# Kernel tuning notes

Measured on AMD Instinct MI355X. Metric: run time of the kernel, lower is better.

Reference implementation:

```python
import jax, jax.numpy as jnp
import numpy as np

B, N_NODES, E = 2, 4096, 16384
H, DQK, DV = 8, 16, 128
DV_HEAD = DV // H  # dim_v_head = dim_v // n_heads


def setup_inputs() -> dict:
    key = jax.random.key(0)
    k1, k2, k3, k4, k5 = jax.random.split(key, 5)
    return {
        "query_values": jax.random.normal(k1, (B, E, H * DQK), jnp.float32),
        "key_values": jax.random.normal(k2, (B, N_NODES, H * DQK), jnp.float32),
        "value_values": jax.random.normal(k3, (B, E, DV), jnp.float32),
        "query_indices": jax.random.randint(k4, (B, E, 2), 0, N_NODES, jnp.int32),
        "value_indices": jax.random.randint(k5, (B, E, 2), 0, N_NODES, jnp.int32),
    }


def _heads(x, d):
    # torch: stack(x.split(d, -1), 0)  => [N, H*d] -> [H, N, d], head-major chunks
    n = x.shape[0]
    return jnp.transpose(x.reshape(n, -1, d), (1, 0, 2))


def reference(query_values, key_values, value_values, query_indices, value_indices):
    b, eq, _ = query_values.shape
    n_nodes = key_values.shape[1]
    n = b * n_nodes                       # total nodes across batch
    nv = b * eq                           # total value/query edges (full mask)
    node_ofs = (jnp.arange(b, dtype=query_indices.dtype) * n_nodes)[:, None, None]

    # _concat_batch: masked flatten (mask all True) + per-head split
    q = _heads(query_values.reshape(nv, -1), DQK)       # [H, Nq, d]
    k = _heads(key_values.reshape(n, -1), DQK)          # [H, n,  d]
    v = _heads(value_values.reshape(nv, -1), DV_HEAD)   # [H, Nv, dv_head]

    # _partial_key_value_sum: gather keys at edge row index, outer product, scatter-add by col
    v_idx = (value_indices + node_ofs).reshape(nv, 2)
    row, col = v_idx[:, 0], v_idx[:, 1]
    k_g = k[:, row, :]                                  # [H, Nv, d]
    # cat(unbind(h),-1).flatten(1,2): layout (n, i*DV + h*DV_HEAD + j)
    kv = jnp.einsum('hni,hnj->nihj', k_g, v).reshape(nv, DQK * DV)
    kg_flat = jnp.transpose(k_g, (1, 0, 2)).reshape(nv, H * DQK)
    kv_k = jnp.concatenate([kv, kg_flat], axis=-1)      # [Nv, DQK*DV + H*DQK]
    kv_k = jax.ops.segment_sum(kv_k, col, num_segments=n)  # coo(...).coalesce().to_dense()

    # _partial_apply_graph_query with dim1=2: gather by query col index
    q_idx = (query_indices + node_ofs).reshape(nv, 2)[:, 1]
    g = kv_k[q_idx]                                     # [Nq, DQK*DV + H*DQK]
    kv_q = jnp.transpose(g[:, :DQK * DV].reshape(nv, DQK, H, DV_HEAD), (2, 0, 1, 3))  # [H,Nq,d,dvh]
    k_sum = jnp.transpose(g[:, DQK * DV:].reshape(nv, H, DQK), (1, 0, 2))             # [H,Nq,d]

    att = jnp.einsum('hni,hnij->hnj', q, kv_q)          # [H, Nq, dv_head]
    qk = jnp.einsum('hni,hni->hn', q, k_sum)[..., None]
    qk = jnp.where(qk == 0, jnp.asarray(1e-5, qk.dtype), qk)
    att = att / qk
    att = jnp.transpose(att, (1, 0, 2)).reshape(b, eq, DV)

    # zero self-loop query edges (ord_q == 2 path)
    loop_mask = (query_indices[..., 0] != query_indices[..., 1])[..., None]
    return jnp.where(loop_mask, att, jnp.zeros((), att.dtype))
```

## Files before the change

### kernel.cpp

```cpp
#include <hip/hip_runtime.h>

#define B_SZ     2
#define E_EDGES  16384
#define N_NODES  4096
#define NTOT     (B_SZ * N_NODES)
#define NV       (B_SZ * E_EDGES)
#define DVTOT    128
#define LOG2_E   14
#define CAP      32

#define ZERO_INT4 200704

__device__ __forceinline__ int padidx(int f) { return f + ((f >> 4) << 2); }

__global__ __launch_bounds__(256) void zero_ws(int4* __restrict__ p) {
    int i = blockIdx.x * blockDim.x + threadIdx.x;
    p[i] = make_int4(0, 0, 0, 0);
}

__global__ __launch_bounds__(256) void fill_all(
    const int* __restrict__ qidx,
    const int* __restrict__ vidx,
    int*  __restrict__ ecnt,
    int*  __restrict__ qcnt,
    int2* __restrict__ ebuf,
    int*  __restrict__ qbuf)
{
    int e = blockIdx.x * blockDim.x + threadIdx.x;
    if (e >= NV) return;
    int ofs = (e >> LOG2_E) * N_NODES;

    int2 vi = ((const int2*)vidx)[e];
    int row = vi.x + ofs;
    int col = vi.y + ofs;
    int p = atomicAdd(&ecnt[col], 1);
    if (p < CAP) ebuf[col * CAP + p] = make_int2(e + 1, row);

    int2 qi = ((const int2*)qidx)[e];
    int g  = qi.y + ofs;
    int pq = atomicAdd(&qcnt[g], 1);
    if (pq < CAP) qbuf[g * CAP + pq] = (e + 1) | ((qi.x == qi.y) ? 0x80000000 : 0);
}

#define KACC(C)                                                          \
    {                                                                    \
        const float4* kp = (const float4*)&sk[wid][C][h20];              \
        float4 k0 = kp[0], k1 = kp[1], k2 = kp[2], k3 = kp[3];           \
        float kk[16] = {k0.x,k0.y,k0.z,k0.w, k1.x,k1.y,k1.z,k1.w,        \
                        k2.x,k2.y,k2.z,k2.w, k3.x,k3.y,k3.z,k3.w};       \
        _Pragma("unroll")                                                \
        for (int i = 0; i < 16; ++i) {                                   \
            ks[i]  += kk[i];                                             \
            kva[i] += kk[i] * vvv[C].x;                                  \
            kvb[i] += kk[i] * vvv[C].y;                                  \
        }                                                                \
    }

#define QOUT(C, TREG)                                                    \
    {                                                                    \
        const float4* qp = (const float4*)&sq[wid][C][h20];              \
        float4 q0 = qp[0], q1 = qp[1], q2 = qp[2], q3 = qp[3];           \
        float qq[16] = {q0.x,q0.y,q0.z,q0.w, q1.x,q1.y,q1.z,q1.w,        \
                        q2.x,q2.y,q2.z,q2.w, q3.x,q3.y,q3.z,q3.w};       \
        float sa = 0.0f, sb = 0.0f, w = 0.0f;                            \
        _Pragma("unroll")                                                \
        for (int i = 0; i < 16; ++i) {                                   \
            sa += qq[i] * kva[i];                                        \
            sb += qq[i] * kvb[i];                                        \
            w  += qq[i] * ks[i];                                         \
        }                                                                \
        float den = (w == 0.0f) ? 1e-5f : w;                             \
        float inv = 1.0f / den;                                          \
        float2 o;                                                        \
        o.x = ((TREG) < 0) ? 0.0f : sa * inv;                            \
        o.y = ((TREG) < 0) ? 0.0f : sb * inv;                            \
        *(float2*)(out + (size_t)(((TREG) & 0x7FFFFFFF) - 1) * DVTOT + f2) = o; \
    }

__global__ __launch_bounds__(256) void attn_node(
    const float* __restrict__ qv,
    const float* __restrict__ keys,
    const float* __restrict__ vals,
    const int2*  __restrict__ ebuf,
    const int*   __restrict__ qbuf,
    float*       __restrict__ out)
{
    __shared__ float sk[4][4][160];
    __shared__ float sq[4][4][160];

    int wid  = threadIdx.x >> 6;
    int lane = threadIdx.x & 63;
    int g    = __builtin_amdgcn_readfirstlane(blockIdx.x * 4 + wid);

    int h20 = (lane >> 3) * 20;
    int f2  = 2 * lane;
    int pf2 = padidx(f2);

    const int2* eb = ebuf + (size_t)g * CAP;
    const int*  qb = qbuf + (size_t)g * CAP;

    int qt[4];
#pragma unroll
    for (int c = 0; c < 4; ++c) qt[c] = qb[c];
    int2 er[4];
#pragma unroll
    for (int c = 0; c < 4; ++c) er[c] = eb[c];

    int nq0 = qt[0] ? (qt[1] ? (qt[2] ? (qt[3] ? 4 : 3) : 2) : 1) : 0;
    if (nq0 == 0) return;
    int dg0 = er[0].x ? (er[1].x ? (er[2].x ? (er[3].x ? 4 : 3) : 2) : 1) : 0;

    float2 kkv[4], vvv[4], qqv[4];
#pragma unroll
    for (int c = 0; c < 4; ++c)
        if (c < dg0) {
            kkv[c] = *(const float2*)(keys + (size_t)er[c].y * DVTOT + f2);
            vvv[c] = *(const float2*)(vals + (size_t)(er[c].x - 1) * DVTOT + f2);
        }
#pragma unroll
    for (int c = 0; c < 4; ++c)
        if (c < nq0)
            qqv[c] = *(const float2*)(qv + (size_t)((qt[c] & 0x7FFFFFFF) - 1) * DVTOT + f2);
#pragma unroll
    for (int c = 0; c < 4; ++c)
        if (c < dg0) *(float2*)&sk[wid][c][pf2] = kkv[c];
#pragma unroll
    for (int c = 0; c < 4; ++c)
        if (c < nq0) *(float2*)&sq[wid][c][pf2] = qqv[c];
    __builtin_amdgcn_wave_barrier();

    float kva[16], kvb[16], ks[16];
#pragma unroll
    for (int i = 0; i < 16; ++i) { kva[i] = 0.0f; kvb[i] = 0.0f; ks[i] = 0.0f; }

#pragma unroll
    for (int c = 0; c < 4; ++c)
        if (c < dg0) KACC(c);

    if (dg0 == 4) {
        for (int base = 4; base < CAP; base += 4) {
            int2 r[4];
#pragma unroll
            for (int c = 0; c < 4; ++c) r[c] = eb[base + c];
            int n = r[0].x ? (r[1].x ? (r[2].x ? (r[3].x ? 4 : 3) : 2) : 1) : 0;
            if (n == 0) break;
#pragma unroll
            for (int c = 0; c < 4; ++c)
                if (c < n) {
                    kkv[c] = *(const float2*)(keys + (size_t)r[c].y * DVTOT + f2);
                    vvv[c] = *(const float2*)(vals + (size_t)(r[c].x - 1) * DVTOT + f2);
                }
            __builtin_amdgcn_wave_barrier();
#pragma unroll
            for (int c = 0; c < 4; ++c)
                if (c < n) *(float2*)&sk[wid][c][pf2] = kkv[c];
            __builtin_amdgcn_wave_barrier();
#pragma unroll
            for (int c = 0; c < 4; ++c)
                if (c < n) KACC(c);
            if (n < 4) break;
        }
    }

#pragma unroll
    for (int c = 0; c < 4; ++c)
        if (c < nq0) QOUT(c, qt[c]);

    if (nq0 == 4) {
        for (int base = 4; base < CAP; base += 4) {
            int t[4];
#pragma unroll
            for (int c = 0; c < 4; ++c) t[c] = qb[base + c];
            int n = t[0] ? (t[1] ? (t[2] ? (t[3] ? 4 : 3) : 2) : 1) : 0;
            if (n == 0) break;
#pragma unroll
            for (int c = 0; c < 4; ++c)
                if (c < n)
                    qqv[c] = *(const float2*)(qv + (size_t)((t[c] & 0x7FFFFFFF) - 1) * DVTOT + f2);
            __builtin_amdgcn_wave_barrier();
#pragma unroll
            for (int c = 0; c < 4; ++c)
                if (c < n) *(float2*)&sq[wid][c][pf2] = qqv[c];
            __builtin_amdgcn_wave_barrier();
#pragma unroll
            for (int c = 0; c < 4; ++c)
                if (c < n) QOUT(c, t[c]);
            if (n < 4) break;
        }
    }
}

extern "C" void kernel_launch(void* const* d_in, const int* in_sizes, int n_in,
                              void* d_out, int out_size, void* d_ws, size_t ws_size,
                              hipStream_t stream) {
    const float* qv   = (const float*)d_in[0];
    const float* keys = (const float*)d_in[1];
    const float* vals = (const float*)d_in[2];
    const int*   qidx = (const int*)d_in[3];
    const int*   vidx = (const int*)d_in[4];
    float* out = (float*)d_out;

    char* ws = (char*)d_ws;
    int*  ecnt = (int*)ws;
    int*  qcnt = ecnt + NTOT;
    int2* ebuf = (int2*)(qcnt + NTOT);
    int*  qbuf = (int*)(ebuf + (size_t)NTOT * CAP);

    zero_ws<<<ZERO_INT4 / 256, 256, 0, stream>>>((int4*)ws);
    fill_all<<<(NV + 255) / 256, 256, 0, stream>>>(qidx, vidx, ecnt, qcnt, ebuf, qbuf);
    attn_node<<<NTOT / 4, 256, 0, stream>>>(qv, keys, vals, ebuf, qbuf, out);
}
```

Baseline: 31.46 us.

## Use per-node counts instead of sentinel-zeroed buckets; split fill into separate threads

Only the per-node counters are zeroed now (16 blocks) rather than the whole bucket workspace, and the attention kernel reads counts to bound its loops instead of scanning for zero sentinels. Edge ids drop the +1 offset. The fill kernel gives value-edge and query-edge insertions to separate threads, doubling the thread count. attn_node gains a launch-bounds occupancy hint of 6 and stores keys directly into LDS. The aim is to remove most of the zeroing traffic and the sentinel reads, with the extra dependency that the count reads stay correct.

```diff
diff --git a/kernel.cpp b/kernel.cpp
--- a/kernel.cpp
+++ b/kernel.cpp
@@ -9,16 +9,14 @@
 #define LOG2_E   14
 #define CAP      32
 
-#define ZERO_INT4 200704
-
 __device__ __forceinline__ int padidx(int f) { return f + ((f >> 4) << 2); }
 
-__global__ __launch_bounds__(256) void zero_ws(int4* __restrict__ p) {
+__global__ __launch_bounds__(256) void zero_counts(int4* __restrict__ p) {
     int i = blockIdx.x * blockDim.x + threadIdx.x;
     p[i] = make_int4(0, 0, 0, 0);
 }
 
-__global__ __launch_bounds__(256) void fill_all(
+__global__ __launch_bounds__(256) void fill_split(
     const int* __restrict__ qidx,
     const int* __restrict__ vidx,
     int*  __restrict__ ecnt,
@@ -26,20 +24,23 @@
     int2* __restrict__ ebuf,
     int*  __restrict__ qbuf)
 {
-    int e = blockIdx.x * blockDim.x + threadIdx.x;
-    if (e >= NV) return;
-    int ofs = (e >> LOG2_E) * N_NODES;
-
-    int2 vi = ((const int2*)vidx)[e];
-    int row = vi.x + ofs;
-    int col = vi.y + ofs;
-    int p = atomicAdd(&ecnt[col], 1);
-    if (p < CAP) ebuf[col * CAP + p] = make_int2(e + 1, row);
-
-    int2 qi = ((const int2*)qidx)[e];
-    int g  = qi.y + ofs;
-    int pq = atomicAdd(&qcnt[g], 1);
-    if (pq < CAP) qbuf[g * CAP + pq] = (e + 1) | ((qi.x == qi.y) ? 0x80000000 : 0);
+    int t = blockIdx.x * blockDim.x + threadIdx.x;
+    if (t < NV) {
+        int e = t;
+        int ofs = (e >> LOG2_E) * N_NODES;
+        int2 vi = ((const int2*)vidx)[e];
+        int row = vi.x + ofs;
+        int col = vi.y + ofs;
+        int p = atomicAdd(&ecnt[col], 1);
+        if (p < CAP) ebuf[col * CAP + p] = make_int2(e, row);
+    } else {
+        int e = t - NV;
+        int ofs = (e >> LOG2_E) * N_NODES;
+        int2 qi = ((const int2*)qidx)[e];
+        int g  = qi.y + ofs;
+        int pq = atomicAdd(&qcnt[g], 1);
+        if (pq < CAP) qbuf[g * CAP + pq] = e | ((qi.x == qi.y) ? 0x80000000 : 0);
+    }
 }
 
 #define KACC(C)                                                          \
@@ -74,13 +75,15 @@
         float2 o;                                                        \
         o.x = ((TREG) < 0) ? 0.0f : sa * inv;                            \
         o.y = ((TREG) < 0) ? 0.0f : sb * inv;                            \
-        *(float2*)(out + (size_t)(((TREG) & 0x7FFFFFFF) - 1) * DVTOT + f2) = o; \
-    }
-
-__global__ __launch_bounds__(256) void attn_node(
+        *(float2*)(out + (size_t)((TREG) & 0x7FFFFFFF) * DVTOT + f2) = o; \
+    }
+
+__global__ __launch_bounds__(256, 6) void attn_node(
     const float* __restrict__ qv,
     const float* __restrict__ keys,
     const float* __restrict__ vals,
+    const int*   __restrict__ ecnt,
+    const int*   __restrict__ qcnt,
     const int2*  __restrict__ ebuf,
     const int*   __restrict__ qbuf,
     float*       __restrict__ out)
@@ -99,34 +102,31 @@
     const int2* eb = ebuf + (size_t)g * CAP;
     const int*  qb = qbuf + (size_t)g * CAP;
 
-    int qt[4];
-#pragma unroll
-    for (int c = 0; c < 4; ++c) qt[c] = qb[c];
-    int2 er[4];
-#pragma unroll
-    for (int c = 0; c < 4; ++c) er[c] = eb[c];
-
-    int nq0 = qt[0] ? (qt[1] ? (qt[2] ? (qt[3] ? 4 : 3) : 2) : 1) : 0;
-    if (nq0 == 0) return;
-    int dg0 = er[0].x ? (er[1].x ? (er[2].x ? (er[3].x ? 4 : 3) : 2) : 1) : 0;
-
-    float2 kkv[4], vvv[4], qqv[4];
+    int nq = qcnt[g];
+    int dg = ecnt[g];
+    int qt[4]; int2 er[4];
+#pragma unroll
+    for (int c = 0; c < 4; ++c) { qt[c] = qb[c]; er[c] = eb[c]; }
+
+    if (nq > CAP) nq = CAP;
+    if (dg > CAP) dg = CAP;
+    if (nq == 0) return;
+    int nq0 = nq < 4 ? nq : 4;
+    int dg0 = dg < 4 ? dg : 4;
+
+    float2 vvv[4];
 #pragma unroll
     for (int c = 0; c < 4; ++c)
         if (c < dg0) {
-            kkv[c] = *(const float2*)(keys + (size_t)er[c].y * DVTOT + f2);
-            vvv[c] = *(const float2*)(vals + (size_t)(er[c].x - 1) * DVTOT + f2);
+            *(float2*)&sk[wid][c][pf2] =
+                *(const float2*)(keys + (size_t)er[c].y * DVTOT + f2);
+            vvv[c] = *(const float2*)(vals + (size_t)er[c].x * DVTOT + f2);
         }
 #pragma unroll
     for (int c = 0; c < 4; ++c)
         if (c < nq0)
-            qqv[c] = *(const float2*)(qv + (size_t)((qt[c] & 0x7FFFFFFF) - 1) * DVTOT + f2);
-#pragma unroll
-    for (int c = 0; c < 4; ++c)
-        if (c < dg0) *(float2*)&sk[wid][c][pf2] = kkv[c];
-#pragma unroll
-    for (int c = 0; c < 4; ++c)
-        if (c < nq0) *(float2*)&sq[wid][c][pf2] = qqv[c];
+            *(float2*)&sq[wid][c][pf2] =
+                *(const float2*)(qv + (size_t)(qt[c] & 0x7FFFFFFF) * DVTOT + f2);
     __builtin_amdgcn_wave_barrier();
 
     float kva[16], kvb[16], ks[16];
@@ -137,56 +137,44 @@
     for (int c = 0; c < 4; ++c)
         if (c < dg0) KACC(c);
 
-    if (dg0 == 4) {
-        for (int base = 4; base < CAP; base += 4) {
-            int2 r[4];
-#pragma unroll
-            for (int c = 0; c < 4; ++c) r[c] = eb[base + c];
-            int n = r[0].x ? (r[1].x ? (r[2].x ? (r[3].x ? 4 : 3) : 2) : 1) : 0;
-            if (n == 0) break;
-#pragma unroll
-            for (int c = 0; c < 4; ++c)
-                if (c < n) {
-                    kkv[c] = *(const float2*)(keys + (size_t)r[c].y * DVTOT + f2);
-                    vvv[c] = *(const float2*)(vals + (size_t)(r[c].x - 1) * DVTOT + f2);
-                }
-            __builtin_amdgcn_wave_barrier();
-#pragma unroll
-            for (int c = 0; c < 4; ++c)
-                if (c < n) *(float2*)&sk[wid][c][pf2] = kkv[c];
-            __builtin_amdgcn_wave_barrier();
-#pragma unroll
-            for (int c = 0; c < 4; ++c)
-                if (c < n) KACC(c);
-            if (n < 4) break;
-        }
+    for (int base = 4; base < dg; base += 4) {
+        int n = dg - base; if (n > 4) n = 4;
+        int2 r[4];
+#pragma unroll
+        for (int c = 0; c < 4; ++c) if (c < n) r[c] = eb[base + c];
+#pragma unroll
+        for (int c = 0; c < 4; ++c)
+            if (c < n) vvv[c] = *(const float2*)(vals + (size_t)r[c].x * DVTOT + f2);
+        __builtin_amdgcn_wave_barrier();
+#pragma unroll
+        for (int c = 0; c < 4; ++c)
+            if (c < n) *(float2*)&sk[wid][c][pf2] =
+                *(const float2*)(keys + (size_t)r[c].y * DVTOT + f2);
+        __builtin_amdgcn_wave_barrier();
+#pragma unroll
+        for (int c = 0; c < 4; ++c) if (c < n) KACC(c);
     }
 
 #pragma unroll
     for (int c = 0; c < 4; ++c)
         if (c < nq0) QOUT(c, qt[c]);
 
-    if (nq0 == 4) {
-        for (int base = 4; base < CAP; base += 4) {
-            int t[4];
-#pragma unroll
-            for (int c = 0; c < 4; ++c) t[c] = qb[base + c];
-            int n = t[0] ? (t[1] ? (t[2] ? (t[3] ? 4 : 3) : 2) : 1) : 0;
-            if (n == 0) break;
-#pragma unroll
-            for (int c = 0; c < 4; ++c)
-                if (c < n)
-                    qqv[c] = *(const float2*)(qv + (size_t)((t[c] & 0x7FFFFFFF) - 1) * DVTOT + f2);
-            __builtin_amdgcn_wave_barrier();
-#pragma unroll
-            for (int c = 0; c < 4; ++c)
-                if (c < n) *(float2*)&sq[wid][c][pf2] = qqv[c];
-            __builtin_amdgcn_wave_barrier();
-#pragma unroll
-            for (int c = 0; c < 4; ++c)
-                if (c < n) QOUT(c, t[c]);
-            if (n < 4) break;
-        }
+    for (int base = 4; base < nq; base += 4) {
+        int n = nq - base; if (n > 4) n = 4;
+        int t[4];
+#pragma unroll
+        for (int c = 0; c < 4; ++c) if (c < n) t[c] = qb[base + c];
+        float2 qv2[4];
+#pragma unroll
+        for (int c = 0; c < 4; ++c)
+            if (c < n) qv2[c] = *(const float2*)(qv + (size_t)(t[c] & 0x7FFFFFFF) * DVTOT + f2);
+        __builtin_amdgcn_wave_barrier();
+#pragma unroll
+        for (int c = 0; c < 4; ++c)
+            if (c < n) *(float2*)&sq[wid][c][pf2] = qv2[c];
+        __builtin_amdgcn_wave_barrier();
+#pragma unroll
+        for (int c = 0; c < 4; ++c) if (c < n) QOUT(c, t[c]);
     }
 }
 
@@ -206,7 +194,7 @@
     int2* ebuf = (int2*)(qcnt + NTOT);
     int*  qbuf = (int*)(ebuf + (size_t)NTOT * CAP);
 
-    zero_ws<<<ZERO_INT4 / 256, 256, 0, stream>>>((int4*)ws);
-    fill_all<<<(NV + 255) / 256, 256, 0, stream>>>(qidx, vidx, ecnt, qcnt, ebuf, qbuf);
-    attn_node<<<NTOT / 4, 256, 0, stream>>>(qv, keys, vals, ebuf, qbuf, out);
-}
+    zero_counts<<<16, 256, 0, stream>>>((int4*)ws);
+    fill_split<<<(2 * NV) / 256, 256, 0, stream>>>(qidx, vidx, ecnt, qcnt, ebuf, qbuf);
+    attn_node<<<NTOT / 4, 256, 0, stream>>>(qv, keys, vals, ecnt, qcnt, ebuf, qbuf, out);
+}
```

Result: slower. 35.00 us (+11.2%).

## Split fill kernel per edge type and prefetch eight bucket entries with branchless loads

Applied to the files above, without the earlier changes.

The fill kernel now uses one thread per value edge or per query edge, doubling the grid so each thread does a single atomic insertion instead of two dependent ones. The attention kernel reads the first eight entries of both the edge and query buckets up front. Its gathers are unconditional, with missing slots clamped to the first valid entry, so loads can be issued together without per-slot branches. This aims to cut serialized latency from index loads and predicated gathers, at the cost of redundant loads, extra registers, and duplicated loop code.

```diff
diff --git a/kernel.cpp b/kernel.cpp
--- a/kernel.cpp
+++ b/kernel.cpp
@@ -18,7 +18,7 @@
     p[i] = make_int4(0, 0, 0, 0);
 }
 
-__global__ __launch_bounds__(256) void fill_all(
+__global__ __launch_bounds__(256) void fill_split(
     const int* __restrict__ qidx,
     const int* __restrict__ vidx,
     int*  __restrict__ ecnt,
@@ -26,23 +26,25 @@
     int2* __restrict__ ebuf,
     int*  __restrict__ qbuf)
 {
-    int e = blockIdx.x * blockDim.x + threadIdx.x;
-    if (e >= NV) return;
-    int ofs = (e >> LOG2_E) * N_NODES;
-
-    int2 vi = ((const int2*)vidx)[e];
-    int row = vi.x + ofs;
-    int col = vi.y + ofs;
-    int p = atomicAdd(&ecnt[col], 1);
-    if (p < CAP) ebuf[col * CAP + p] = make_int2(e + 1, row);
-
-    int2 qi = ((const int2*)qidx)[e];
-    int g  = qi.y + ofs;
-    int pq = atomicAdd(&qcnt[g], 1);
-    if (pq < CAP) qbuf[g * CAP + pq] = (e + 1) | ((qi.x == qi.y) ? 0x80000000 : 0);
-}
-
-#define KACC(C)                                                          \
+    int t = blockIdx.x * blockDim.x + threadIdx.x;
+    if (t < NV) {
+        int e = t;
+        int ofs = (e >> LOG2_E) * N_NODES;
+        int2 vi = ((const int2*)vidx)[e];
+        int col = vi.y + ofs;
+        int p = atomicAdd(&ecnt[col], 1);
+        if (p < CAP) ebuf[col * CAP + p] = make_int2(e + 1, vi.x + ofs);
+    } else {
+        int e = t - NV;
+        int ofs = (e >> LOG2_E) * N_NODES;
+        int2 qi = ((const int2*)qidx)[e];
+        int g  = qi.y + ofs;
+        int pq = atomicAdd(&qcnt[g], 1);
+        if (pq < CAP) qbuf[g * CAP + pq] = (e + 1) | ((qi.x == qi.y) ? 0x80000000 : 0);
+    }
+}
+
+#define KACC(C, V)                                                       \
     {                                                                    \
         const float4* kp = (const float4*)&sk[wid][C][h20];              \
         float4 k0 = kp[0], k1 = kp[1], k2 = kp[2], k3 = kp[3];           \
@@ -51,8 +53,8 @@
         _Pragma("unroll")                                                \
         for (int i = 0; i < 16; ++i) {                                   \
             ks[i]  += kk[i];                                             \
-            kva[i] += kk[i] * vvv[C].x;                                  \
-            kvb[i] += kk[i] * vvv[C].y;                                  \
+            kva[i] += kk[i] * (V).x;                                     \
+            kvb[i] += kk[i] * (V).y;                                     \
         }                                                                \
     }
 
@@ -99,66 +101,87 @@
     const int2* eb = ebuf + (size_t)g * CAP;
     const int*  qb = qbuf + (size_t)g * CAP;
 
-    int qt[4];
-#pragma unroll
-    for (int c = 0; c < 4; ++c) qt[c] = qb[c];
-    int2 er[4];
-#pragma unroll
-    for (int c = 0; c < 4; ++c) er[c] = eb[c];
+    int qt[8]; int2 er[8];
+#pragma unroll
+    for (int c = 0; c < 8; ++c) { qt[c] = qb[c]; er[c] = eb[c]; }
 
     int nq0 = qt[0] ? (qt[1] ? (qt[2] ? (qt[3] ? 4 : 3) : 2) : 1) : 0;
     if (nq0 == 0) return;
     int dg0 = er[0].x ? (er[1].x ? (er[2].x ? (er[3].x ? 4 : 3) : 2) : 1) : 0;
 
-    float2 kkv[4], vvv[4], qqv[4];
+    float2 vvv[4];
+    if (dg0) {
+#pragma unroll
+        for (int c = 0; c < 4; ++c) {
+            int2 rc = (c < dg0) ? er[c] : er[0];
+            *(float2*)&sk[wid][c][pf2] =
+                *(const float2*)(keys + (size_t)rc.y * DVTOT + f2);
+            vvv[c] = *(const float2*)(vals + (size_t)(rc.x - 1) * DVTOT + f2);
+        }
+    }
+#pragma unroll
+    for (int c = 0; c < 4; ++c) {
+        int tc = (c < nq0) ? qt[c] : qt[0];
+        *(float2*)&sq[wid][c][pf2] =
+            *(const float2*)(qv + (size_t)((tc & 0x7FFFFFFF) - 1) * DVTOT + f2);
+    }
+    __builtin_amdgcn_wave_barrier();
+
+    float kva[16], kvb[16], ks[16];
+#pragma unroll
+    for (int i = 0; i < 16; ++i) { kva[i] = 0.0f; kvb[i] = 0.0f; ks[i] = 0.0f; }
+
 #pragma unroll
     for (int c = 0; c < 4; ++c)
-        if (c < dg0) {
-            kkv[c] = *(const float2*)(keys + (size_t)er[c].y * DVTOT + f2);
-            vvv[c] = *(const float2*)(vals + (size_t)(er[c].x - 1) * DVTOT + f2);
-        }
-#pragma unroll
-    for (int c = 0; c < 4; ++c)
-        if (c < nq0)
-            qqv[c] = *(const float2*)(qv + (size_t)((qt[c] & 0x7FFFFFFF) - 1) * DVTOT + f2);
-#pragma unroll
-    for (int c = 0; c < 4; ++c)
-        if (c < dg0) *(float2*)&sk[wid][c][pf2] = kkv[c];
-#pragma unroll
-    for (int c = 0; c < 4; ++c)
-        if (c < nq0) *(float2*)&sq[wid][c][pf2] = qqv[c];
-    __builtin_amdgcn_wave_barrier();
-
-    float kva[16], kvb[16], ks[16];
-#pragma unroll
-    for (int i = 0; i < 16; ++i) { kva[i] = 0.0f; kvb[i] = 0.0f; ks[i] = 0.0f; }
-
-#pragma unroll
-    for (int c = 0; c < 4; ++c)
-        if (c < dg0) KACC(c);
+        if (c < dg0) KACC(c, vvv[c]);
 
     if (dg0 == 4) {
-        for (int base = 4; base < CAP; base += 4) {
-            int2 r[4];
-#pragma unroll
-            for (int c = 0; c < 4; ++c) r[c] = eb[base + c];
-            int n = r[0].x ? (r[1].x ? (r[2].x ? (r[3].x ? 4 : 3) : 2) : 1) : 0;
-            if (n == 0) break;
+        int n1 = er[4].x ? (er[5].x ? (er[6].x ? (er[7].x ? 4 : 3) : 2) : 1) : 0;
+        if (n1) {
+            float2 vv[4];
+#pragma unroll
+            for (int c = 0; c < 4; ++c) {
+                int2 rc = (c < n1) ? er[4 + c] : er[4];
+                vv[c] = *(const float2*)(vals + (size_t)(rc.x - 1) * DVTOT + f2);
+            }
+            __builtin_amdgcn_wave_barrier();
+#pragma unroll
+            for (int c = 0; c < 4; ++c) {
+                int2 rc = (c < n1) ? er[4 + c] : er[4];
+                *(float2*)&sk[wid][c][pf2] =
+                    *(const float2*)(keys + (size_t)rc.y * DVTOT + f2);
+            }
+            __builtin_amdgcn_wave_barrier();
 #pragma unroll
             for (int c = 0; c < 4; ++c)
-                if (c < n) {
-                    kkv[c] = *(const float2*)(keys + (size_t)r[c].y * DVTOT + f2);
-                    vvv[c] = *(const float2*)(vals + (size_t)(r[c].x - 1) * DVTOT + f2);
+                if (c < n1) KACC(c, vv[c]);
+            if (n1 == 4) {
+                for (int base = 8; base < CAP; base += 4) {
+                    int2 r[4];
+#pragma unroll
+                    for (int c = 0; c < 4; ++c) r[c] = eb[base + c];
+                    int n = r[0].x ? (r[1].x ? (r[2].x ? (r[3].x ? 4 : 3) : 2) : 1) : 0;
+                    if (n == 0) break;
+                    float2 vr[4];
+#pragma unroll
+                    for (int c = 0; c < 4; ++c) {
+                        int2 rc = (c < n) ? r[c] : r[0];
+                        vr[c] = *(const float2*)(vals + (size_t)(rc.x - 1) * DVTOT + f2);
+                    }
+                    __builtin_amdgcn_wave_barrier();
+#pragma unroll
+                    for (int c = 0; c < 4; ++c) {
+                        int2 rc = (c < n) ? r[c] : r[0];
+                        *(float2*)&sk[wid][c][pf2] =
+                            *(const float2*)(keys + (size_t)rc.y * DVTOT + f2);
+                    }
+                    __builtin_amdgcn_wave_barrier();
+#pragma unroll
+                    for (int c = 0; c < 4; ++c)
+                        if (c < n) KACC(c, vr[c]);
+                    if (n < 4) break;
                 }
-            __builtin_amdgcn_wave_barrier();
-#pragma unroll
-            for (int c = 0; c < 4; ++c)
-                if (c < n) *(float2*)&sk[wid][c][pf2] = kkv[c];
-            __builtin_amdgcn_wave_barrier();
-#pragma unroll
-            for (int c = 0; c < 4; ++c)
-                if (c < n) KACC(c);
-            if (n < 4) break;
+            }
         }
     }
 
@@ -167,25 +190,46 @@
         if (c < nq0) QOUT(c, qt[c]);
 
     if (nq0 == 4) {
-        for (int base = 4; base < CAP; base += 4) {
-            int t[4];
-#pragma unroll
-            for (int c = 0; c < 4; ++c) t[c] = qb[base + c];
-            int n = t[0] ? (t[1] ? (t[2] ? (t[3] ? 4 : 3) : 2) : 1) : 0;
-            if (n == 0) break;
+        int n1 = qt[4] ? (qt[5] ? (qt[6] ? (qt[7] ? 4 : 3) : 2) : 1) : 0;
+        if (n1) {
+            float2 q2[4];
+#pragma unroll
+            for (int c = 0; c < 4; ++c) {
+                int tc = (c < n1) ? qt[4 + c] : qt[4];
+                q2[c] = *(const float2*)(qv + (size_t)((tc & 0x7FFFFFFF) - 1) * DVTOT + f2);
+            }
+            __builtin_amdgcn_wave_barrier();
 #pragma unroll
             for (int c = 0; c < 4; ++c)
-                if (c < n)
-                    qqv[c] = *(const float2*)(qv + (size_t)((t[c] & 0x7FFFFFFF) - 1) * DVTOT + f2);
+                *(float2*)&sq[wid][c][pf2] = q2[c];
             __builtin_amdgcn_wave_barrier();
 #pragma unroll
             for (int c = 0; c < 4; ++c)
-                if (c < n) *(float2*)&sq[wid][c][pf2] = qqv[c];
-            __builtin_amdgcn_wave_barrier();
-#pragma unroll
-            for (int c = 0; c < 4; ++c)
-                if (c < n) QOUT(c, t[c]);
-            if (n < 4) break;
+                if (c < n1) QOUT(c, qt[4 + c]);
+            if (n1 == 4) {
+                for (int base = 8; base < CAP; base += 4) {
+                    int t[4];
+#pragma unroll
+                    for (int c = 0; c < 4; ++c) t[c] = qb[base + c];
+                    int n = t[0] ? (t[1] ? (t[2] ? (t[3] ? 4 : 3) : 2) : 1) : 0;
+                    if (n == 0) break;
+                    float2 qr[4];
+#pragma unroll
+                    for (int c = 0; c < 4; ++c) {
+                        int tc = (c < n) ? t[c] : t[0];
+                        qr[c] = *(const float2*)(qv + (size_t)((tc & 0x7FFFFFFF) - 1) * DVTOT + f2);
+                    }
+                    __builtin_amdgcn_wave_barrier();
+#pragma unroll
+                    for (int c = 0; c < 4; ++c)
+                        *(float2*)&sq[wid][c][pf2] = qr[c];
+                    __builtin_amdgcn_wave_barrier();
+#pragma unroll
+                    for (int c = 0; c < 4; ++c)
+                        if (c < n) QOUT(c, t[c]);
+                    if (n < 4) break;
+                }
+            }
         }
     }
 }
@@ -207,6 +251,6 @@
     int*  qbuf = (int*)(ebuf + (size_t)NTOT * CAP);
 
     zero_ws<<<ZERO_INT4 / 256, 256, 0, stream>>>((int4*)ws);
-    fill_all<<<(NV + 255) / 256, 256, 0, stream>>>(qidx, vidx, ecnt, qcnt, ebuf, qbuf);
+    fill_split<<<(2 * NV) / 256, 256, 0, stream>>>(qidx, vidx, ecnt, qcnt, ebuf, qbuf);
     attn_node<<<NTOT / 4, 256, 0, stream>>>(qv, keys, vals, ebuf, qbuf, out);
 }
```

Measured after the change: 30.91 us. No clear change (-1.8%).
